# Kernel tuning notes

Hardware: AMD Instinct MI355X
Metric: run time of the kernel (lower is better)

## Reference

```python
import jax, jax.numpy as jnp
import numpy as np

N_SAMPLES = 8_000_000
NB_CLASSES = 5


def setup_inputs() -> dict:
    key = jax.random.key(0)
    k1, k2 = jax.random.split(key)
    preds = jax.random.normal(k1, (N_SAMPLES, NB_CLASSES), dtype=jnp.float32)
    true = jax.random.randint(k2, (N_SAMPLES,), 0, NB_CLASSES, dtype=jnp.int32)
    return {"preds": preds, "true": true}


def reference(preds, true):
    N, C = preds.shape
    dt = preds.dtype
    cls = jnp.arange(C, dtype=dt)

    # SoftArgmax1D per row (base_index=0, step_size=1), then round -> hard class
    soft_arg = jax.nn.softmax(preds, axis=1) @ cls            # [N]
    pred_idx = jnp.clip(jnp.round(soft_arg).astype(jnp.int32), 0, C - 1)

    # confusion_matrix[true, pred] += 1 via fused scatter-add on flat index
    flat = true * C + pred_idx                                 # [N]
    conf = jnp.zeros((C * C,), dtype=dt).at[flat].add(1.0).reshape(C, C)

    # quadratic kappa weights: (i-j)^2 / (C-1)^2
    weights = (cls[:, None] - cls[None, :]) ** 2 / ((C - 1) ** 2)

    # class histograms (scatter-add)
    true_hist = jnp.zeros((C,), dtype=dt).at[true].add(1.0)
    pred_hist = jnp.zeros((C,), dtype=dt).at[pred_idx].add(1.0)

    # expected matrix E = outer(true_hist, pred_hist), both normalized
    E = jnp.outer(true_hist, pred_hist)
    E = E / E.sum()
    conf = conf / conf.sum()

    num = (conf * weights).sum()
    den = (E * weights).sum()
    return num / den
```

## Files before the change

### kernel.cpp

```cpp
#include <hip/hip_runtime.h>
#include <math.h>

#define NCLS 5
#define NBINS 25
#define NTHREADS 256
#define NBLOCKS 4096

__global__ void __launch_bounds__(NTHREADS, 4)
kappa_count(const float* __restrict__ preds,
            const int* __restrict__ truev,
            int N,
            unsigned int* __restrict__ partials) {
    __shared__ unsigned int s_conf[4 * 32];
    const int tid = threadIdx.x;
    const int wv = tid >> 6;
    if (tid < 128) s_conf[tid] = 0u;
    __syncthreads();
    unsigned int* hist = &s_conf[wv << 5];

    auto dorow = [&](float r0, float r1, float r2, float r3, float r4, int t) {
        float m = fmaxf(fmaxf(fmaxf(fmaxf(r0, r1), r2), r3), r4);
        float e0 = __expf(r0 - m), e1 = __expf(r1 - m), e2 = __expf(r2 - m),
              e3 = __expf(r3 - m), e4 = __expf(r4 - m);
        float s = e0 + e1 + e2 + e3 + e4;
        float dot = e1 + e2 * 2.f + e3 * 3.f + e4 * 4.f;
        int pi = (int)rintf(dot / s);
        pi = min(max(pi, 0), NCLS - 1);
        atomicAdd(&hist[t * NCLS + pi], 1u);
    };

    const int nquad = N >> 2;
    const int gs = gridDim.x * blockDim.x;

    int q = blockIdx.x * blockDim.x + tid;
    if (q < nquad) {
        const float4* p4 = (const float4*)preds + (size_t)q * 5u;
        float4 a = p4[0], b = p4[1], c = p4[2], d = p4[3], e = p4[4];
        int4 t4 = *(const int4*)(truev + (size_t)q * 4u);
        for (;;) {
            const int qn = q + gs;
            const bool more = qn < nquad;
            float4 an, bn, cn, dn, en;
            int4 tn;
            if (more) {
                const float4* pn = (const float4*)preds + (size_t)qn * 5u;
                an = pn[0]; bn = pn[1]; cn = pn[2]; dn = pn[3]; en = pn[4];
                tn = *(const int4*)(truev + (size_t)qn * 4u);
            }
            dorow(a.x, a.y, a.z, a.w, b.x, t4.x);
            dorow(b.y, b.z, b.w, c.x, c.y, t4.y);
            dorow(c.z, c.w, d.x, d.y, d.z, t4.z);
            dorow(d.w, e.x, e.y, e.z, e.w, t4.w);
            if (!more) break;
            a = an; b = bn; c = cn; d = dn; e = en; t4 = tn;
            q = qn;
        }
    }

    if (blockIdx.x == 0 && tid < (N & 3)) {
        const int i = (N & ~3) + tid;
        float v[NCLS];
        #pragma unroll
        for (int j = 0; j < NCLS; j++) v[j] = preds[(size_t)i * NCLS + j];
        dorow(v[0], v[1], v[2], v[3], v[4], truev[i]);
    }

    __syncthreads();
    if (tid < NBINS) {
        unsigned int v = s_conf[tid] + s_conf[32 + tid] +
                         s_conf[64 + tid] + s_conf[96 + tid];
        partials[(size_t)tid * gridDim.x + blockIdx.x] = v;
    }
}

__global__ void kappa_final(const unsigned int* __restrict__ partials,
                            int nb,
                            float* __restrict__ out) {
    __shared__ double s_bin[NBINS];
    const int tid = threadIdx.x;
    const int bin = tid >> 5;
    const int l = tid & 31;

    if (bin < NBINS) {
        unsigned int acc = 0u;
        const unsigned int* p = partials + (size_t)bin * nb;
        for (int j = l; j < nb; j += 32) acc += p[j];
        #pragma unroll
        for (int off = 16; off > 0; off >>= 1)
            acc += __shfl_down(acc, off, 32);
        if (l == 0) s_bin[bin] = (double)acc;
    }
    __syncthreads();

    if (tid == 0) {
        double tot = 0.0;
        for (int i = 0; i < NBINS; i++) tot += s_bin[i];
        double th[NCLS] = {0, 0, 0, 0, 0};
        double ph[NCLS] = {0, 0, 0, 0, 0};
        for (int i = 0; i < NCLS; i++)
            for (int j = 0; j < NCLS; j++) {
                th[i] += s_bin[i * NCLS + j];
                ph[j] += s_bin[i * NCLS + j];
            }
        double num = 0.0, den = 0.0;
        for (int i = 0; i < NCLS; i++)
            for (int j = 0; j < NCLS; j++) {
                double w = (double)((i - j) * (i - j)) / 16.0;
                num += w * s_bin[i * NCLS + j];
                den += w * th[i] * ph[j];
            }
        out[0] = (float)(num * tot / den);
    }
}

extern "C" void kernel_launch(void* const* d_in, const int* in_sizes, int n_in,
                              void* d_out, int out_size, void* d_ws, size_t ws_size,
                              hipStream_t stream) {
    const float* preds = (const float*)d_in[0];
    const int* truev = (const int*)d_in[1];
    const int N = in_sizes[1];

    int nblocks = NBLOCKS;
    size_t need = (size_t)nblocks * NBINS * sizeof(unsigned int);
    if (need > ws_size) nblocks = (int)(ws_size / (NBINS * sizeof(unsigned int)));
    unsigned int* partials = (unsigned int*)d_ws;

    kappa_count<<<nblocks, NTHREADS, 0, stream>>>(preds, truev, N, partials);
    kappa_final<<<1, 1024, 0, stream>>>(partials, nblocks, (float*)d_out);
}
```

Measured before the change: 259.5 us.

## Stage per-wave chunks into LDS with async global_load_lds double buffering

Replaces the per-thread float4 register prefetch with per-wavefront chunks of 256 rows, copied into LDS using global_load_lds (direct-to-LDS DMA) and double-buffered with s_waitcnt vmcnt. Rows are then read from LDS with a stride of 5 floats per lane. The grid shrinks from 4096 to 768 blocks and the occupancy hint in launch bounds is dropped. The goal is more bytes in flight with fully coalesced loads and fewer VGPRs, at the cost of LDS bank conflicts on the strided reads. There is also a risk in relying on hand-written vmcnt counts and on no wave-level barrier being needed before reading the LDS data.

```diff
diff --git a/kernel.cpp b/kernel.cpp
--- a/kernel.cpp
+++ b/kernel.cpp
@@ -4,19 +4,47 @@
 #define NCLS 5
 #define NBINS 25
 #define NTHREADS 256
-#define NBLOCKS 4096
+#define NBLOCKS 768
+#define ROWS_PER_CHUNK 256
+#define CHUNK_PRED_F4 320
+#define PRED_SEGS 5
 
-__global__ void __launch_bounds__(NTHREADS, 4)
+__device__ __forceinline__ void gload_lds16(const void* g, void* l) {
+    __builtin_amdgcn_global_load_lds(
+        (const __attribute__((address_space(1))) unsigned int*)(const unsigned int*)g,
+        (__attribute__((address_space(3))) unsigned int*)(unsigned int*)l,
+        16, 0, 0);
+}
+
+__global__ void __launch_bounds__(NTHREADS)
 kappa_count(const float* __restrict__ preds,
             const int* __restrict__ truev,
             int N,
             unsigned int* __restrict__ partials) {
+    __shared__ float s_pred[2][4][ROWS_PER_CHUNK * NCLS];
+    __shared__ int   s_lab [2][4][ROWS_PER_CHUNK];
     __shared__ unsigned int s_conf[4 * 32];
+
     const int tid = threadIdx.x;
     const int wv = tid >> 6;
+    const int lane = tid & 63;
     if (tid < 128) s_conf[tid] = 0u;
     __syncthreads();
     unsigned int* hist = &s_conf[wv << 5];
+
+    const int nchunks = N / ROWS_PER_CHUNK;
+    const int wgid = blockIdx.x * 4 + wv;
+    const int wstride = gridDim.x * 4;
+
+    auto stage = [&](int c, int b) {
+        const float4* sp = (const float4*)preds + (size_t)c * CHUNK_PRED_F4;
+        #pragma unroll
+        for (int k = 0; k < PRED_SEGS; ++k)
+            gload_lds16(sp + k * 64 + lane,
+                        &s_pred[b][wv][k * 256]);
+        const int4* sl = (const int4*)(truev + (size_t)c * ROWS_PER_CHUNK);
+        gload_lds16(sl + lane, &s_lab[b][wv][0]);
+    };
 
     auto dorow = [&](float r0, float r1, float r2, float r3, float r4, int t) {
         float m = fmaxf(fmaxf(fmaxf(fmaxf(r0, r1), r2), r3), r4);
@@ -29,48 +57,42 @@
         atomicAdd(&hist[t * NCLS + pi], 1u);
     };
 
-    const int nquad = N >> 2;
-    const int gs = gridDim.x * blockDim.x;
+    int c = wgid, cur = 0;
+    if (c < nchunks) stage(c, 0);
+    for (; c < nchunks; c += wstride) {
+        const int cn = c + wstride;
+        if (cn < nchunks) {
+            stage(cn, cur ^ 1);
+            asm volatile("s_waitcnt vmcnt(6)" ::: "memory");
+        } else {
+            asm volatile("s_waitcnt vmcnt(0)" ::: "memory");
+        }
+        const float* bp = s_pred[cur][wv];
+        const int* lp = s_lab[cur][wv];
+        #pragma unroll
+        for (int rr = 0; rr < 4; ++rr) {
+            const int r = lane + (rr << 6);
+            const float* rp = bp + r * NCLS;
+            dorow(rp[0], rp[1], rp[2], rp[3], rp[4], lp[r]);
+        }
+        cur ^= 1;
+    }
 
-    int q = blockIdx.x * blockDim.x + tid;
-    if (q < nquad) {
-        const float4* p4 = (const float4*)preds + (size_t)q * 5u;
-        float4 a = p4[0], b = p4[1], c = p4[2], d = p4[3], e = p4[4];
-        int4 t4 = *(const int4*)(truev + (size_t)q * 4u);
-        for (;;) {
-            const int qn = q + gs;
-            const bool more = qn < nquad;
-            float4 an, bn, cn, dn, en;
-            int4 tn;
-            if (more) {
-                const float4* pn = (const float4*)preds + (size_t)qn * 5u;
-                an = pn[0]; bn = pn[1]; cn = pn[2]; dn = pn[3]; en = pn[4];
-                tn = *(const int4*)(truev + (size_t)qn * 4u);
-            }
-            dorow(a.x, a.y, a.z, a.w, b.x, t4.x);
-            dorow(b.y, b.z, b.w, c.x, c.y, t4.y);
-            dorow(c.z, c.w, d.x, d.y, d.z, t4.z);
-            dorow(d.w, e.x, e.y, e.z, e.w, t4.w);
-            if (!more) break;
-            a = an; b = bn; c = cn; d = dn; e = en; t4 = tn;
-            q = qn;
+    if (blockIdx.x == 0 && wv == 0) {
+        for (int r = nchunks * ROWS_PER_CHUNK + lane; r < N; r += 64) {
+            float v0 = preds[(size_t)r * NCLS + 0];
+            float v1 = preds[(size_t)r * NCLS + 1];
+            float v2 = preds[(size_t)r * NCLS + 2];
+            float v3 = preds[(size_t)r * NCLS + 3];
+            float v4 = preds[(size_t)r * NCLS + 4];
+            dorow(v0, v1, v2, v3, v4, truev[r]);
         }
     }
 
-    if (blockIdx.x == 0 && tid < (N & 3)) {
-        const int i = (N & ~3) + tid;
-        float v[NCLS];
-        #pragma unroll
-        for (int j = 0; j < NCLS; j++) v[j] = preds[(size_t)i * NCLS + j];
-        dorow(v[0], v[1], v[2], v[3], v[4], truev[i]);
-    }
-
     __syncthreads();
-    if (tid < NBINS) {
-        unsigned int v = s_conf[tid] + s_conf[32 + tid] +
-                         s_conf[64 + tid] + s_conf[96 + tid];
-        partials[(size_t)tid * gridDim.x + blockIdx.x] = v;
-    }
+    if (tid < NBINS)
+        partials[(size_t)tid * gridDim.x + blockIdx.x] =
+            s_conf[tid] + s_conf[32 + tid] + s_conf[64 + tid] + s_conf[96 + tid];
 }
 
 __global__ void kappa_final(const unsigned int* __restrict__ partials,
```

Measured after the change: 246.5 us. 1.05x faster.
